# Kernel optimization log

Measured on AMD Instinct MI355X. Metric: run time of the kernel, lower is better.

## Reference

```python
import jax, jax.numpy as jnp
import numpy as np

# dims
B, T, C, D, H, NH, HD, INTER, L = 4, 1024, 256, 256, 512, 8, 64, 2048, 4
CF, CB, BASE = 0, 128, 10000.0  # context_forward, context_backward, rope theta


def _rope_tables():
    inv = 1.0 / (BASE ** (jnp.arange(0, HD, 2, dtype=jnp.float32) / HD))
    t = jnp.arange(T, dtype=jnp.float32)
    f = jnp.einsum('i,j->ij', t, inv)          # [T, HD/2]
    emb = jnp.concatenate([f, f], axis=-1)      # [T, HD]
    return jnp.cos(emb), jnp.sin(emb)


def _rotate_half(x):
    x1, x2 = jnp.split(x, 2, axis=-1)
    return jnp.concatenate([-x2, x1], axis=-1)


def _ln(x, g, b):
    m = x.mean(-1, keepdims=True)
    v = ((x - m) ** 2).mean(-1, keepdims=True)
    return (x - m) / jnp.sqrt(v + 1e-5) * g + b


def _band_mask():
    # create_context_mask(CF, CB, T): allow j in [i-CB, i+CF]
    i = jnp.arange(T)[:, None]
    j = jnp.arange(T)[None, :]
    return (j <= i + CF) & (j >= i - CB)  # [T, T] bool


def setup_inputs() -> dict:
    key = jax.random.key(0)
    ks = jax.random.split(key, 16)
    w = lambda k, shp: (0.02 * jax.random.normal(k, shp)).astype(jnp.float32)
    return {
        'spikes': jax.random.normal(ks[0], (B, T, C), dtype=jnp.float32),
        'spikes_mask': jnp.ones((B, T), dtype=jnp.int32),
        'spikes_timestamp': jnp.tile(jnp.arange(T, dtype=jnp.int32), (B, 1)),
        'embed_w': w(ks[1], (C, D)), 'embed_b': jnp.zeros((D,), jnp.float32),
        'proj_w': w(ks[2], (D, H)), 'proj_b': jnp.zeros((H,), jnp.float32),
        'ln1_g': jnp.ones((L, H), jnp.float32), 'ln1_b': jnp.zeros((L, H), jnp.float32),
        'Wq': w(ks[3], (L, H, H)), 'bq': jnp.zeros((L, H), jnp.float32),
        'Wk': w(ks[4], (L, H, H)), 'bk': jnp.zeros((L, H), jnp.float32),
        'Wv': w(ks[5], (L, H, H)), 'bv': jnp.zeros((L, H), jnp.float32),
        'Wo': w(ks[6], (L, H, H)), 'bo': jnp.zeros((L, H), jnp.float32),
        'ln2_g': jnp.ones((L, H), jnp.float32), 'ln2_b': jnp.zeros((L, H), jnp.float32),
        'up_w': w(ks[7], (L, H, INTER)), 'up_b': jnp.zeros((L, INTER), jnp.float32),
        'down_w': w(ks[8], (L, INTER, H)), 'down_b': jnp.zeros((L, H), jnp.float32),
    }


def reference(spikes, spikes_mask, spikes_timestamp, embed_w, embed_b, proj_w, proj_b,
              ln1_g, ln1_b, Wq, bq, Wk, bk, Wv, bv, Wo, bo, ln2_g, ln2_b,
              up_w, up_b, down_w, down_b):
    cos, sin = _rope_tables()
    mask = _band_mask()[None, None] & (spikes_mask[:, None, None, :] > 0)  # [B,1,T,T]
    cs = cos[spikes_timestamp][:, None]  # [B,1,T,HD]
    sn = sin[spikes_timestamp][:, None]
    neg = jnp.finfo(jnp.float32).min

    # NeuralEmbeddingLayer (no stack/pos/tokens): Linear -> gelu -> Linear
    x = jax.nn.gelu(spikes @ embed_w + embed_b, approximate=False) @ proj_w + proj_b

    for l in range(L):
        h = _ln(x, ln1_g[l], ln1_b[l])
        q = (h @ Wq[l] + bq[l]).reshape(B, T, NH, HD).transpose(0, 2, 1, 3)
        k = (h @ Wk[l] + bk[l]).reshape(B, T, NH, HD).transpose(0, 2, 1, 3)
        v = (h @ Wv[l] + bv[l]).reshape(B, T, NH, HD).transpose(0, 2, 1, 3)
        q = q * cs + _rotate_half(q) * sn
        k = k * cs + _rotate_half(k) * sn
        s = jnp.einsum('bhqd,bhkd->bhqk', q, k) / np.float32(np.sqrt(HD))
        s = jnp.where(mask, s, neg)
        p = jax.nn.softmax(s, axis=-1)
        o = jnp.einsum('bhqk,bhkd->bhqd', p, v).transpose(0, 2, 1, 3).reshape(B, T, H)
        x = x + o @ Wo[l] + bo[l]
        h = _ln(x, ln2_g[l], ln2_b[l])
        x = x + jax.nn.gelu(h @ up_w[l] + up_b[l], approximate=False) @ down_w[l] + down_b[l]
    return x
```

## Files before the change

kernel.cpp:

```cpp
#include <hip/hip_runtime.h>
#include <math.h>

#define B_ 4
#define T_ 1024
#define C_ 256
#define D_ 256
#define H_ 512
#define NH_ 8
#define HD_ 64
#define INTER_ 2048
#define L_ 4
#define CB_ 128

typedef short bf16x8 __attribute__((ext_vector_type(8)));
typedef unsigned short ush8 __attribute__((ext_vector_type(8)));
typedef float f32x4 __attribute__((ext_vector_type(4)));

__device__ __forceinline__ float gelu_exact(float x) {
    return 0.5f * x * (1.0f + erff(x * 0.70710678118654752f));
}

__device__ __forceinline__ unsigned short f2bf(float f) {
    unsigned u = __float_as_uint(f);
    u += 0x7fffu + ((u >> 16) & 1u);
    return (unsigned short)(u >> 16);
}
__device__ __forceinline__ float bf2f(unsigned short h) {
    return __uint_as_float((unsigned)h << 16);
}

__device__ __forceinline__ void xcd_swz(int& bx, int& by) {
    const int gx  = gridDim.x;
    const int nwg = gx * gridDim.y;
    int bid = blockIdx.y * gx + blockIdx.x;
    bid = (bid & 7) * (nwg >> 3) + (bid >> 3);
    bx = bid % gx;
    by = bid / gx;
}

template<int ACT, int RES, int OBF, int SPLIT>
__global__ __launch_bounds__(256) void mm64_k(
    const unsigned short* __restrict__ A, const unsigned short* __restrict__ BT,
    const float* __restrict__ b0, const float* __restrict__ b1,
    const float* __restrict__ b2,
    const float* res,
    void* o0, void* o1, void* o2,
    const int M, const int N, const int K)
{
    __shared__ unsigned short As[64 * 256];
    __shared__ unsigned short Bs[64 * 256];

    int bx, by; xcd_swz(bx, by);

    const int tid  = threadIdx.x;
    const int lane = tid & 63;
    const int w    = tid >> 6;
    const int m0   = by * 64;
    const int n0   = bx * 64;
    const int wm   = (w >> 1) * 32;
    const int wn   = (w & 1) * 32;
    const int l16  = lane & 15;
    const int g16  = lane >> 4;

    f32x4 acc[2][2] = {};

    const unsigned short* Abase = A  + (size_t)m0 * K;
    const unsigned short* Bbase = BT + (size_t)n0 * K;

    for (int k0 = 0; k0 < K; k0 += 256) {
        __syncthreads();
#pragma unroll
        for (int it = 0; it < 8; ++it) {
            const int c  = it * 256 + tid;
            const int rc = c >> 5;
            const int gk = (c & 31) ^ (rc & 7);
            __builtin_amdgcn_global_load_lds(
                (const __attribute__((address_space(1))) unsigned*)(Abase + (size_t)rc * K + k0 + gk * 8),
                (__attribute__((address_space(3))) unsigned*)(As + (size_t)(it * 256 + (w << 6)) * 8), 16, 0, 0);
        }
#pragma unroll
        for (int it = 0; it < 8; ++it) {
            const int c  = it * 256 + tid;
            const int rc = c >> 5;
            const int gk = (c & 31) ^ (rc & 7);
            __builtin_amdgcn_global_load_lds(
                (const __attribute__((address_space(1))) unsigned*)(Bbase + (size_t)rc * K + k0 + gk * 8),
                (__attribute__((address_space(3))) unsigned*)(Bs + (size_t)(it * 256 + (w << 6)) * 8), 16, 0, 0);
        }
        __syncthreads();

#pragma unroll
        for (int kk = 0; kk < 8; ++kk) {
            const int kf = kk * 4 + g16;
            const int sw = (kf ^ (l16 & 7)) * 8;
            bf16x8 a[2], b[2];
#pragma unroll
            for (int t = 0; t < 2; ++t)
                a[t] = *(const bf16x8*)&As[(wm + t * 16 + l16) * 256 + sw];
#pragma unroll
            for (int t = 0; t < 2; ++t)
                b[t] = *(const bf16x8*)&Bs[(wn + t * 16 + l16) * 256 + sw];
#pragma unroll
            for (int i = 0; i < 2; ++i)
#pragma unroll
                for (int j = 0; j < 2; ++j)
                    acc[i][j] = __builtin_amdgcn_mfma_f32_16x16x32_bf16(a[i], b[j], acc[i][j], 0, 0, 0);
        }
    }

    if (OBF || SPLIT) {
        __syncthreads();
        unsigned short* Eb = ((w < 2) ? As : Bs) + (w & 1) * 1024;
        const int row16 = lane >> 2;
        const int cg    = lane & 3;

        const int gnb   = n0 + wn;
        const int which = SPLIT ? (gnb >> 9) : 0;
        const int lnb   = SPLIT ? (gnb & 511) : gnb;
        const int ldo   = SPLIT ? 512 : N;
        unsigned short* oo = SPLIT
            ? ((which == 0) ? (unsigned short*)o0 : (which == 1) ? (unsigned short*)o1 : (unsigned short*)o2)
            : (unsigned short*)o0;
        const float* bb = SPLIT ? ((which == 0) ? b0 : (which == 1) ? b1 : b2) : b0;
        const float scale = (SPLIT && which == 0) ? 0.125f : 1.0f;

#pragma unroll
        for (int i = 0; i < 2; ++i) {
#pragma unroll
            for (int j = 0; j < 2; ++j) {
                const float bv = bb[lnb + j * 16 + l16];
#pragma unroll
                for (int r = 0; r < 4; ++r) {
                    float cv = acc[i][j][r] + bv;
                    if (ACT) cv = gelu_exact(cv);
                    if (SPLIT) cv *= scale;
                    Eb[(g16 * 4 + r) * 40 + j * 16 + l16] = f2bf(cv);
                }
            }
            const int grow0 = m0 + wm + i * 16 + row16;
#pragma unroll
            for (int s = 0; s < 2; ++s) {
                ushort4 t4 = *(const ushort4*)&Eb[row16 * 40 + s * 16 + cg * 4];
                *(ushort4*)&oo[(size_t)grow0 * ldo + lnb + s * 16 + cg * 4] = t4;
            }
        }
        return;
    }

#pragma unroll
    for (int i = 0; i < 2; ++i) {
        const int gmb = m0 + wm + i * 16 + g16 * 4;
#pragma unroll
        for (int j = 0; j < 2; ++j) {
            const int gn = n0 + wn + j * 16 + l16;
            const float bv = b0[gn];
#pragma unroll
            for (int r = 0; r < 4; ++r) {
                float cv = acc[i][j][r] + bv;
                if (ACT) cv = gelu_exact(cv);
                if (RES) cv += res[(size_t)(gmb + r) * 512 + gn];
                ((float*)o0)[(size_t)(gmb + r) * N + gn] = cv;
            }
        }
    }
}

template<int ACT, int RES, int OBF, int SPLIT, int BN>
__global__ __launch_bounds__(256) void mm128_k(
    const unsigned short* __restrict__ A, const unsigned short* __restrict__ BT,
    const float* __restrict__ b0, const float* __restrict__ b1,
    const float* __restrict__ b2,
    const float* res,
    void* o0, void* o1, void* o2,
    const int M, const int N, const int K)
{
    constexpr int NJ = BN / 32;

    __shared__ unsigned short As[128 * 128];
    __shared__ unsigned short Bs[BN * 128];

    int bx, by; xcd_swz(bx, by);

    const int tid  = threadIdx.x;
    const int lane = tid & 63;
    const int w    = tid >> 6;
    const int m0   = by * 128;
    const int n0   = bx * BN;
    const int wm   = (w >> 1) * 64;
    const int wn   = (w & 1) * (BN / 2);
    const int l16  = lane & 15;
    const int g16  = lane >> 4;

    f32x4 acc[4][NJ] = {};

    const unsigned short* Abase = A  + (size_t)m0 * K;
    const unsigned short* Bbase = BT + (size_t)n0 * K;

    for (int k0 = 0; k0 < K; k0 += 128) {
        __syncthreads();
#pragma unroll
        for (int it = 0; it < 8; ++it) {
            const int c  = it * 256 + tid;
            const int rc = c >> 4;
            const int gk = (c & 15) ^ (rc & 7);
            __builtin_amdgcn_global_load_lds(
                (const __attribute__((address_space(1))) unsigned*)(Abase + (size_t)rc * K + k0 + gk * 8),
                (__attribute__((address_space(3))) unsigned*)(As + (size_t)(it * 256 + (w << 6)) * 8), 16, 0, 0);
        }
#pragma unroll
        for (int it = 0; it < NJ * 2; ++it) {
            const int c  = it * 256 + tid;
            const int rc = c >> 4;
            const int gk = (c & 15) ^ (rc & 7);
            __builtin_amdgcn_global_load_lds(
                (const __attribute__((address_space(1))) unsigned*)(Bbase + (size_t)rc * K + k0 + gk * 8),
                (__attribute__((address_space(3))) unsigned*)(Bs + (size_t)(it * 256 + (w << 6)) * 8), 16, 0, 0);
        }
        __syncthreads();

#pragma unroll
        for (int kk = 0; kk < 4; ++kk) {
            const int kf = kk * 4 + g16;
            const int sw = (kf ^ (l16 & 7)) * 8;
            bf16x8 a[4], b[NJ];
#pragma unroll
            for (int t = 0; t < 4; ++t)
                a[t] = *(const bf16x8*)&As[(wm + t * 16 + l16) * 128 + sw];
#pragma unroll
            for (int t = 0; t < NJ; ++t)
                b[t] = *(const bf16x8*)&Bs[(wn + t * 16 + l16) * 128 + sw];
#pragma unroll
            for (int i = 0; i < 4; ++i)
#pragma unroll
                for (int j = 0; j < NJ; ++j)
                    acc[i][j] = __builtin_amdgcn_mfma_f32_16x16x32_bf16(a[i], b[j], acc[i][j], 0, 0, 0);
        }
    }

    if (OBF || SPLIT) {
        __syncthreads();
        constexpr int WC  = NJ * 16;
        constexpr int EST = WC + 8;
        constexpr int LPR = WC / 4;
        constexpr int RPI = 64 / LPR;
        unsigned short* Eb = As + w * (16 * EST);
        const int erow = lane / LPR;
        const int ecol = (lane % LPR) * 4;

        const int gnb   = n0 + wn;
        const int which = SPLIT ? (gnb >> 9) : 0;
        const int lnb   = SPLIT ? (gnb & 511) : gnb;
        const int ldo   = SPLIT ? 512 : N;
        unsigned short* oo = SPLIT
            ? ((which == 0) ? (unsigned short*)o0 : (which == 1) ? (unsigned short*)o1 : (unsigned short*)o2)
            : (unsigned short*)o0;
        const float* bb = SPLIT ? ((which == 0) ? b0 : (which == 1) ? b1 : b2) : b0;
        const float scale = (SPLIT && which == 0) ? 0.125f : 1.0f;

#pragma unroll
        for (int i = 0; i < 4; ++i) {
#pragma unroll
            for (int j = 0; j < NJ; ++j) {
                const float bv = bb[lnb + j * 16 + l16];
#pragma unroll
                for (int r = 0; r < 4; ++r) {
                    float cv = acc[i][j][r] + bv;
                    if (ACT) cv = gelu_exact(cv);
                    if (SPLIT) cv *= scale;
                    Eb[(g16 * 4 + r) * EST + j * 16 + l16] = f2bf(cv);
                }
            }
            const int grow0 = m0 + wm + i * 16;
#pragma unroll
            for (int s = 0; s < NJ; ++s) {
                ushort4 t4 = *(const ushort4*)&Eb[(s * RPI + erow) * EST + ecol];
                *(ushort4*)&oo[(size_t)(grow0 + s * RPI + erow) * ldo + lnb + ecol] = t4;
            }
        }
        return;
    }

#pragma unroll
    for (int i = 0; i < 4; ++i) {
        const int gmb = m0 + wm + i * 16 + g16 * 4;
#pragma unroll
        for (int j = 0; j < NJ; ++j) {
            const int gn = n0 + wn + j * 16 + l16;
            const float bv = b0[gn];
#pragma unroll
            for (int r = 0; r < 4; ++r) {
                float cv = acc[i][j][r] + bv;
                if (ACT) cv = gelu_exact(cv);
                if (RES) cv += res[(size_t)(gmb + r) * 512 + gn];
                ((float*)o0)[(size_t)(gmb + r) * N + gn] = cv;
            }
        }
    }
}

__global__ __launch_bounds__(256) void prep_k(
    const float* __restrict__ spikes,
    const float* __restrict__ embed_w, const float* __restrict__ proj_w,
    const float* __restrict__ Wq, const float* __restrict__ Wk,
    const float* __restrict__ Wv, const float* __restrict__ Wo,
    const float* __restrict__ up_w, const float* __restrict__ down_w,
    const int* __restrict__ ts,
    unsigned short* __restrict__ spbf,
    unsigned short* __restrict__ embT, unsigned short* __restrict__ projT,
    unsigned short* __restrict__ qkvT, unsigned short* __restrict__ woT,
    unsigned short* __restrict__ upT, unsigned short* __restrict__ downT,
    float2* __restrict__ rope_tab)
{
    const int idx = blockIdx.x;
    const int tid = threadIdx.x;

    if (idx >= 3376) {
        const int e0 = (idx - 3376) * 4096 + tid * 16;
#pragma unroll
        for (int i = 0; i < 16; ++i) {
            const int e = e0 + i;
            const int row = e >> 5, d = e & 31;
            const float tstamp = (float)ts[row];
            const float freq = __expf(-0.2878231366242558f * (float)d);
            const float ang = tstamp * freq;
            rope_tab[e] = make_float2(__cosf(ang), __sinf(ang));
        }
        return;
    }

    if (idx >= 3120) {
        const int base = (idx - 3120) * 4096 + tid * 16;
#pragma unroll
        for (int s = 0; s < 4; ++s) {
            float4 v = *(const float4*)&spikes[base + s * 4];
            ushort4 o = {f2bf(v.x), f2bf(v.y), f2bf(v.z), f2bf(v.w)};
            *(ushort4*)&spbf[base + s * 4] = o;
        }
        return;
    }

    const float* src; unsigned short* dst; int R, Cc, t;
    if (idx < 16)      { src = embed_w; dst = embT;  R = C_; Cc = D_; t = idx; }
    else if (idx < 48) { src = proj_w;  dst = projT; R = D_; Cc = H_; t = idx - 16; }
    else if (idx < 816) {
        const int j = idx - 48;
        const int wsel = j >> 8;
        const int l = (j & 255) >> 6;
        t = j & 63;
        src = ((wsel == 0) ? Wq : (wsel == 1) ? Wk : Wv) + (size_t)l * H_ * H_;
        dst = qkvT + (size_t)l * 3 * H_ * H_ + (size_t)wsel * H_ * H_;
        R = H_; Cc = H_;
    } else if (idx < 1072) {
        const int j = idx - 816; const int l = j >> 6; t = j & 63;
        src = Wo + (size_t)l * H_ * H_; dst = woT + (size_t)l * H_ * H_;
        R = H_; Cc = H_;
    } else if (idx < 2096) {
        const int j = idx - 1072; const int l = j >> 8; t = j & 255;
        src = up_w + (size_t)l * H_ * INTER_; dst = upT + (size_t)l * INTER_ * H_;
        R = H_; Cc = INTER_;
    } else {
        const int j = idx - 2096; const int l = j >> 8; t = j & 255;
        src = down_w + (size_t)l * INTER_ * H_; dst = downT + (size_t)l * H_ * INTER_;
        R = INTER_; Cc = H_;
    }
    const int ntx = Cc >> 6;
    const int c0 = (t % ntx) * 64, r0 = (t / ntx) * 64;

    __shared__ float tile[64][65];
    const int tr = tid >> 4, tc = (tid & 15) * 4;
#pragma unroll
    for (int i = 0; i < 4; ++i) {
        float4 v = *(const float4*)&src[(size_t)(r0 + tr + i * 16) * Cc + c0 + tc];
        tile[tr + i * 16][tc + 0] = v.x;
        tile[tr + i * 16][tc + 1] = v.y;
        tile[tr + i * 16][tc + 2] = v.z;
        tile[tr + i * 16][tc + 3] = v.w;
    }
    __syncthreads();
#pragma unroll
    for (int i = 0; i < 4; ++i) {
        const int n = tr + i * 16;
        ushort4 o;
        o.x = f2bf(tile[tc + 0][n]);
        o.y = f2bf(tile[tc + 1][n]);
        o.z = f2bf(tile[tc + 2][n]);
        o.w = f2bf(tile[tc + 3][n]);
        *(ushort4*)&dst[(size_t)(c0 + n) * R + r0 + tc] = o;
    }
}

__global__ __launch_bounds__(256) void ln_k(
    const float* __restrict__ x, const float* __restrict__ g,
    const float* __restrict__ b, unsigned short* __restrict__ out)
{
    const int wave = threadIdx.x >> 6;
    const int lane = threadIdx.x & 63;
    const int row  = blockIdx.x * 4 + wave;
    const float* xr = x + (size_t)row * H_;
    const int c0 = lane * 8;

    float4 a0 = *(const float4*)&xr[c0];
    float4 a1 = *(const float4*)&xr[c0 + 4];

    float s = a0.x + a0.y + a0.z + a0.w + a1.x + a1.y + a1.z + a1.w;
#pragma unroll
    for (int off = 32; off; off >>= 1) s += __shfl_xor(s, off);
    const float mean = s * (1.0f / (float)H_);

    float d[8];
    d[0] = a0.x - mean; d[1] = a0.y - mean; d[2] = a0.z - mean; d[3] = a0.w - mean;
    d[4] = a1.x - mean; d[5] = a1.y - mean; d[6] = a1.z - mean; d[7] = a1.w - mean;
    float q = 0.0f;
#pragma unroll
    for (int j = 0; j < 8; ++j) q += d[j] * d[j];
#pragma unroll
    for (int off = 32; off; off >>= 1) q += __shfl_xor(q, off);
    const float rstd = rsqrtf(q * (1.0f / (float)H_) + 1e-5f);

    float4 g0 = *(const float4*)&g[c0];
    float4 g1 = *(const float4*)&g[c0 + 4];
    float4 b0 = *(const float4*)&b[c0];
    float4 b1 = *(const float4*)&b[c0 + 4];

    ushort4 o0, o1;
    o0.x = f2bf(d[0] * rstd * g0.x + b0.x);
    o0.y = f2bf(d[1] * rstd * g0.y + b0.y);
    o0.z = f2bf(d[2] * rstd * g0.z + b0.z);
    o0.w = f2bf(d[3] * rstd * g0.w + b0.w);
    o1.x = f2bf(d[4] * rstd * g1.x + b1.x);
    o1.y = f2bf(d[5] * rstd * g1.y + b1.y);
    o1.z = f2bf(d[6] * rstd * g1.z + b1.z);
    o1.w = f2bf(d[7] * rstd * g1.w + b1.w);
    *(ushort4*)&out[(size_t)row * H_ + c0]     = o0;
    *(ushort4*)&out[(size_t)row * H_ + c0 + 4] = o1;
}

#define AWIN 192
#define AKS 72
#define AVS 200

__global__ __launch_bounds__(256) void attn_k(
    const unsigned short* __restrict__ q, const unsigned short* __restrict__ k,
    const unsigned short* __restrict__ v, const int* __restrict__ smask,
    const float2* __restrict__ rope_tab, unsigned short* __restrict__ o)
{
    __shared__ unsigned short Ks[AWIN * AKS];
    __shared__ unsigned short Vt[64 * AVS];
    unsigned short* const Pb = Ks;

    const int blk = blockIdx.x;
    const int qt = blk & 15;
    const int h  = (blk >> 4) & 7;
    const int b  = blk >> 7;
    const int tid  = threadIdx.x;
    const int lane = tid & 63;
    const int w    = tid >> 6;
    const int l16  = lane & 15;
    const int g16  = lane >> 4;

    const int qlo = qt * 64;
    const int klo = (qlo >= CB_) ? (qlo - CB_) : 0;
    const int tb  = b * 1024;

    bf16x8 qa0, qa1;
    {
        const int qrow = w * 16 + l16;
        const unsigned short* gq = q + ((size_t)(tb + qlo + qrow)) * 512 + h * 64;
        ush8 lo = *(const ush8*)&gq[g16 * 8];
        ush8 hi = *(const ush8*)&gq[g16 * 8 + 32];
        const float2* tr = rope_tab + (size_t)(tb + qlo + qrow) * 32 + g16 * 8;
#pragma unroll
        for (int j = 0; j < 8; ++j) {
            const float2 cs = tr[j];
            const float v1 = bf2f(lo[j]);
            const float v2 = bf2f(hi[j]);
            ((unsigned short*)&qa0)[j] = f2bf(v1 * cs.x - v2 * cs.y);
            ((unsigned short*)&qa1)[j] = f2bf(v2 * cs.x + v1 * cs.y);
        }
    }

    {
        const unsigned short* gk = k + ((size_t)(tb + klo)) * 512 + h * 64;
        for (int c = tid; c < AWIN * 8; c += 256) {
            const int row = c >> 3, c4 = (c & 7) * 4;
            ushort4 lo = *(const ushort4*)&gk[(size_t)row * 512 + c4];
            ushort4 hi = *(const ushort4*)&gk[(size_t)row * 512 + c4 + 32];
            const float2* tr = rope_tab + (size_t)(tb + klo + row) * 32 + c4;
            ushort4 olo, ohi;
#pragma unroll
            for (int j2 = 0; j2 < 4; ++j2) {
                const float2 cs = tr[j2];
                const float v1 = bf2f(((const unsigned short*)&lo)[j2]);
                const float v2 = bf2f(((const unsigned short*)&hi)[j2]);
                ((unsigned short*)&olo)[j2] = f2bf(v1 * cs.x - v2 * cs.y);
                ((unsigned short*)&ohi)[j2] = f2bf(v2 * cs.x + v1 * cs.y);
            }
            *(ushort4*)&Ks[row * AKS + c4]      = olo;
            *(ushort4*)&Ks[row * AKS + c4 + 32] = ohi;
        }
    }
    {
        const unsigned short* gv = v + ((size_t)(tb + klo)) * 512 + h * 64;
        for (int c = tid; c < AWIN * 16; c += 256) {
            const int row = c >> 4, c4 = (c & 15) * 4;
            ushort4 vv = *(const ushort4*)&gv[(size_t)row * 512 + c4];
            Vt[(c4 + 0) * AVS + row] = vv.x;
            Vt[(c4 + 1) * AVS + row] = vv.y;
            Vt[(c4 + 2) * AVS + row] = vv.z;
            Vt[(c4 + 3) * AVS + row] = vv.w;
        }
    }
    __syncthreads();

    f32x4 accs[12];
#pragma unroll
    for (int t = 0; t < 12; ++t) {
        const bf16x8 b0 = *(const bf16x8*)&Ks[(t * 16 + l16) * AKS + g16 * 8];
        const bf16x8 b1 = *(const bf16x8*)&Ks[(t * 16 + l16) * AKS + 32 + g16 * 8];
        f32x4 c = {};
        c = __builtin_amdgcn_mfma_f32_16x16x32_bf16(qa0, b0, c, 0, 0, 0);
        c = __builtin_amdgcn_mfma_f32_16x16x32_bf16(qa1, b1, c, 0, 0, 0);
        accs[t] = c;
    }

    bool mk[12];
    int  jj[12];
#pragma unroll
    for (int t = 0; t < 12; ++t) {
        jj[t] = klo + t * 16 + l16;
        mk[t] = smask[tb + jj[t]] > 0;
    }

    float rs[4];
#pragma unroll
    for (int r = 0; r < 4; ++r) {
        const int i = qlo + 16 * w + g16 * 4 + r;
        float mx = -1e30f;
#pragma unroll
        for (int t = 0; t < 12; ++t) {
            const bool val = mk[t] && (jj[t] >= i - CB_) && (jj[t] <= i);
            mx = fmaxf(mx, val ? accs[t][r] : -1e30f);
        }
        mx = fmaxf(mx, __shfl_xor(mx, 1));
        mx = fmaxf(mx, __shfl_xor(mx, 2));
        mx = fmaxf(mx, __shfl_xor(mx, 4));
        mx = fmaxf(mx, __shfl_xor(mx, 8));
        float sum = 0.0f;
#pragma unroll
        for (int t = 0; t < 12; ++t) {
            const bool val = mk[t] && (jj[t] >= i - CB_) && (jj[t] <= i);
            const float p = val ? __expf(accs[t][r] - mx) : 0.0f;
            accs[t][r] = p;
            sum += p;
        }
        sum += __shfl_xor(sum, 1);
        sum += __shfl_xor(sum, 2);
        sum += __shfl_xor(sum, 4);
        sum += __shfl_xor(sum, 8);
        rs[r] = 1.0f / sum;
    }

    __syncthreads();

#pragma unroll
    for (int t = 0; t < 12; ++t)
#pragma unroll
        for (int r = 0; r < 4; ++r)
            Pb[(16 * w + g16 * 4 + r) * AVS + t * 16 + l16] = f2bf(accs[t][r]);

    f32x4 acco[4];
#pragma unroll
    for (int nt = 0; nt < 4; ++nt) {
        f32x4 c = {};
#pragma unroll
        for (int ks = 0; ks < 6; ++ks) {
            const bf16x8 a = *(const bf16x8*)&Pb[(16 * w + l16) * AVS + ks * 32 + g16 * 8];
            const bf16x8 bb = *(const bf16x8*)&Vt[(nt * 16 + l16) * AVS + ks * 32 + g16 * 8];
            c = __builtin_amdgcn_mfma_f32_16x16x32_bf16(a, bb, c, 0, 0, 0);
        }
        acco[nt] = c;
    }

    __syncthreads();
#pragma unroll
    for (int nt = 0; nt < 4; ++nt)
#pragma unroll
        for (int r = 0; r < 4; ++r)
            Pb[(16 * w + g16 * 4 + r) * AVS + nt * 16 + l16] = f2bf(acco[nt][r] * rs[r]);

    const int row16 = lane >> 2, cg = lane & 3;
    const int grow = tb + qlo + 16 * w + row16;
#pragma unroll
    for (int s = 0; s < 4; ++s) {
        ushort4 t4 = *(const ushort4*)&Pb[(16 * w + row16) * AVS + s * 16 + cg * 4];
        *(ushort4*)&o[(size_t)grow * 512 + h * 64 + s * 16 + cg * 4] = t4;
    }
}

extern "C" void kernel_launch(void* const* d_in, const int* in_sizes, int n_in,
                              void* d_out, int out_size, void* d_ws, size_t ws_size,
                              hipStream_t stream)
{
    const float* spikes  = (const float*)d_in[0];
    const int*   smask   = (const int*)d_in[1];
    const int*   ts      = (const int*)d_in[2];
    const float* embed_w = (const float*)d_in[3];
    const float* embed_b = (const float*)d_in[4];
    const float* proj_w  = (const float*)d_in[5];
    const float* proj_b  = (const float*)d_in[6];
    const float* ln1_g   = (const float*)d_in[7];
    const float* ln1_b   = (const float*)d_in[8];
    const float* Wq      = (const float*)d_in[9];
    const float* bq      = (const float*)d_in[10];
    const float* Wk      = (const float*)d_in[11];
    const float* bk      = (const float*)d_in[12];
    const float* Wv      = (const float*)d_in[13];
    const float* bv      = (const float*)d_in[14];
    const float* Wo      = (const float*)d_in[15];
    const float* bo      = (const float*)d_in[16];
    const float* ln2_g   = (const float*)d_in[17];
    const float* ln2_b   = (const float*)d_in[18];
    const float* up_w    = (const float*)d_in[19];
    const float* up_b    = (const float*)d_in[20];
    const float* down_w  = (const float*)d_in[21];
    const float* down_b  = (const float*)d_in[22];

    const int M = B_ * T_;

    char* p = (char*)d_ws;
    float* x = (float*)p;                       p += (size_t)M * H_ * 4;
    unsigned short* qb  = (unsigned short*)p;   p += (size_t)M * H_ * 2;
    unsigned short* kb  = (unsigned short*)p;   p += (size_t)M * H_ * 2;
    unsigned short* vb  = (unsigned short*)p;   p += (size_t)M * H_ * 2;
    unsigned short* hbf = (unsigned short*)p;   p += (size_t)M * H_ * 2;
    unsigned short* obf = (unsigned short*)p;   p += (size_t)M * H_ * 2;
    unsigned short* ibf = (unsigned short*)p;   p += (size_t)M * INTER_ * 2;
    unsigned short* tbf = (unsigned short*)p;   p += (size_t)M * D_ * 2;
    unsigned short* spbf  = (unsigned short*)p; p += (size_t)M * C_ * 2;
    unsigned short* embT  = (unsigned short*)p; p += (size_t)D_ * C_ * 2;
    unsigned short* projT = (unsigned short*)p; p += (size_t)H_ * D_ * 2;
    unsigned short* qkvT  = (unsigned short*)p; p += (size_t)L_ * 3 * H_ * H_ * 2;
    unsigned short* woT   = (unsigned short*)p; p += (size_t)L_ * H_ * H_ * 2;
    unsigned short* upT   = (unsigned short*)p; p += (size_t)L_ * INTER_ * H_ * 2;
    unsigned short* downT = (unsigned short*)p; p += (size_t)L_ * H_ * INTER_ * 2;
    float2* rope_tab = (float2*)p;              p += (size_t)M * 32 * sizeof(float2);

    prep_k<<<3408, 256, 0, stream>>>(
        spikes, embed_w, proj_w, Wq, Wk, Wv, Wo, up_w, down_w, ts,
        spbf, embT, projT, qkvT, woT, upT, downT, rope_tab);

    mm64_k<1, 0, 1, 0><<<dim3(D_ / 64, M / 64), 256, 0, stream>>>(
        spbf, embT, embed_b, nullptr, nullptr, nullptr,
        tbf, nullptr, nullptr, M, D_, C_);
    mm64_k<0, 0, 0, 0><<<dim3(H_ / 64, M / 64), 256, 0, stream>>>(
        tbf, projT, proj_b, nullptr, nullptr, nullptr,
        x, nullptr, nullptr, M, H_, D_);

    for (int l = 0; l < L_; ++l) {
        const unsigned short* qkvT_l = qkvT + (size_t)l * 3 * H_ * H_;
        const unsigned short* woT_l  = woT  + (size_t)l * H_ * H_;
        const unsigned short* upT_l  = upT  + (size_t)l * INTER_ * H_;
        const unsigned short* dnT_l  = downT + (size_t)l * H_ * INTER_;

        ln_k<<<M / 4, 256, 0, stream>>>(x, ln1_g + l * H_, ln1_b + l * H_, hbf);

        mm128_k<0, 0, 1, 1, 64><<<dim3((3 * H_) / 64, M / 128), 256, 0, stream>>>(
            hbf, qkvT_l, bq + l * H_, bk + l * H_, bv + l * H_, nullptr,
            qb, kb, vb, M, 3 * H_, H_);

        attn_k<<<B_ * NH_ * (T_ / 64), 256, 0, stream>>>(qb, kb, vb, smask,
                                                         rope_tab, obf);

        mm64_k<0, 1, 0, 0><<<dim3(H_ / 64, M / 64), 256, 0, stream>>>(
            obf, woT_l, bo + l * H_, nullptr, nullptr, x,
            x, nullptr, nullptr, M, H_, H_);

        ln_k<<<M / 4, 256, 0, stream>>>(x, ln2_g + l * H_, ln2_b + l * H_, hbf);

        mm128_k<1, 0, 1, 0, 128><<<dim3(INTER_ / 128, M / 128), 256, 0, stream>>>(
            hbf, upT_l, up_b + l * INTER_, nullptr, nullptr, nullptr,
            ibf, nullptr, nullptr, M, INTER_, H_);

        float* dst = (l == L_ - 1) ? (float*)d_out : x;
        mm64_k<0, 1, 0, 0><<<dim3(H_ / 64, M / 64), 256, 0, stream>>>(
            ibf, dnT_l, down_b + l * H_, nullptr, nullptr, x,
            dst, nullptr, nullptr, M, H_, INTER_);
    }
}
```

Measured before the change: 483.5 us.

## Fuse RoPE into QKV GEMM epilogue and drop it from attention

RoPE is now applied in the QKV projection epilogue. Each warp is remapped to own 32 rows by all 64 columns of a head, so the rotate-half partner columns sit in the same thread's accumulators. The attention kernel then loads already-rotated Q and K straight from global memory, skipping the per-block rotation and the rope table reads. This removes RoPE work that was repeated across overlapping attention windows, at the cost of a different warp tiling and more epilogue work in the QKV GEMM.

```diff
diff --git a/kernel.cpp b/kernel.cpp
--- a/kernel.cpp
+++ b/kernel.cpp
@@ -38,13 +38,12 @@
     by = bid / gx;
 }
 
-template<int ACT, int RES, int OBF, int SPLIT>
+template<int ACT, int RES, int OBF>
 __global__ __launch_bounds__(256) void mm64_k(
     const unsigned short* __restrict__ A, const unsigned short* __restrict__ BT,
-    const float* __restrict__ b0, const float* __restrict__ b1,
-    const float* __restrict__ b2,
+    const float* __restrict__ b0,
     const float* res,
-    void* o0, void* o1, void* o2,
+    void* o0,
     const int M, const int N, const int K)
 {
     __shared__ unsigned short As[64 * 256];
@@ -108,32 +107,21 @@
         }
     }
 
-    if (OBF || SPLIT) {
+    if (OBF) {
         __syncthreads();
         unsigned short* Eb = ((w < 2) ? As : Bs) + (w & 1) * 1024;
         const int row16 = lane >> 2;
         const int cg    = lane & 3;
 
-        const int gnb   = n0 + wn;
-        const int which = SPLIT ? (gnb >> 9) : 0;
-        const int lnb   = SPLIT ? (gnb & 511) : gnb;
-        const int ldo   = SPLIT ? 512 : N;
-        unsigned short* oo = SPLIT
-            ? ((which == 0) ? (unsigned short*)o0 : (which == 1) ? (unsigned short*)o1 : (unsigned short*)o2)
-            : (unsigned short*)o0;
-        const float* bb = SPLIT ? ((which == 0) ? b0 : (which == 1) ? b1 : b2) : b0;
-        const float scale = (SPLIT && which == 0) ? 0.125f : 1.0f;
-
 #pragma unroll
         for (int i = 0; i < 2; ++i) {
 #pragma unroll
             for (int j = 0; j < 2; ++j) {
-                const float bv = bb[lnb + j * 16 + l16];
+                const float bv = b0[n0 + wn + j * 16 + l16];
 #pragma unroll
                 for (int r = 0; r < 4; ++r) {
                     float cv = acc[i][j][r] + bv;
                     if (ACT) cv = gelu_exact(cv);
-                    if (SPLIT) cv *= scale;
                     Eb[(g16 * 4 + r) * 40 + j * 16 + l16] = f2bf(cv);
                 }
             }
@@ -141,7 +129,7 @@
 #pragma unroll
             for (int s = 0; s < 2; ++s) {
                 ushort4 t4 = *(const ushort4*)&Eb[row16 * 40 + s * 16 + cg * 4];
-                *(ushort4*)&oo[(size_t)grow0 * ldo + lnb + s * 16 + cg * 4] = t4;
+                *(ushort4*)&((unsigned short*)o0)[(size_t)grow0 * N + n0 + wn + s * 16 + cg * 4] = t4;
             }
         }
         return;
@@ -165,16 +153,17 @@
     }
 }
 
-template<int ACT, int RES, int OBF, int SPLIT, int BN>
+template<int ACT, int OBF, int SPLIT, int BN>
 __global__ __launch_bounds__(256) void mm128_k(
     const unsigned short* __restrict__ A, const unsigned short* __restrict__ BT,
     const float* __restrict__ b0, const float* __restrict__ b1,
     const float* __restrict__ b2,
-    const float* res,
+    const float2* __restrict__ rope_tab,
     void* o0, void* o1, void* o2,
     const int M, const int N, const int K)
 {
-    constexpr int NJ = BN / 32;
+    constexpr int NI = SPLIT ? 2 : 4;
+    constexpr int NJ = SPLIT ? 4 : (BN / 32);
 
     __shared__ unsigned short As[128 * 128];
     __shared__ unsigned short Bs[BN * 128];
@@ -186,12 +175,12 @@
     const int w    = tid >> 6;
     const int m0   = by * 128;
     const int n0   = bx * BN;
-    const int wm   = (w >> 1) * 64;
-    const int wn   = (w & 1) * (BN / 2);
+    const int wm   = SPLIT ? (w * 32) : ((w >> 1) * 64);
+    const int wn   = SPLIT ? 0 : ((w & 1) * (BN / 2));
     const int l16  = lane & 15;
     const int g16  = lane >> 4;
 
-    f32x4 acc[4][NJ] = {};
+    f32x4 acc[NI][NJ] = {};
 
     const unsigned short* Abase = A  + (size_t)m0 * K;
     const unsigned short* Bbase = BT + (size_t)n0 * K;
@@ -208,7 +197,7 @@
                 (__attribute__((address_space(3))) unsigned*)(As + (size_t)(it * 256 + (w << 6)) * 8), 16, 0, 0);
         }
 #pragma unroll
-        for (int it = 0; it < NJ * 2; ++it) {
+        for (int it = 0; it < (BN / 128) * 8 + (BN == 64 ? 4 : 0); ++it) {
             const int c  = it * 256 + tid;
             const int rc = c >> 4;
             const int gk = (c & 15) ^ (rc & 7);
@@ -222,22 +211,69 @@
         for (int kk = 0; kk < 4; ++kk) {
             const int kf = kk * 4 + g16;
             const int sw = (kf ^ (l16 & 7)) * 8;
-            bf16x8 a[4], b[NJ];
-#pragma unroll
-            for (int t = 0; t < 4; ++t)
+            bf16x8 a[NI], b[NJ];
+#pragma unroll
+            for (int t = 0; t < NI; ++t)
                 a[t] = *(const bf16x8*)&As[(wm + t * 16 + l16) * 128 + sw];
 #pragma unroll
             for (int t = 0; t < NJ; ++t)
                 b[t] = *(const bf16x8*)&Bs[(wn + t * 16 + l16) * 128 + sw];
 #pragma unroll
-            for (int i = 0; i < 4; ++i)
+            for (int i = 0; i < NI; ++i)
 #pragma unroll
                 for (int j = 0; j < NJ; ++j)
                     acc[i][j] = __builtin_amdgcn_mfma_f32_16x16x32_bf16(a[i], b[j], acc[i][j], 0, 0, 0);
         }
     }
 
-    if (OBF || SPLIT) {
+    if (SPLIT) {
+        __syncthreads();
+        constexpr int EST = 72;
+        unsigned short* Eb = As + w * (16 * EST);
+        const int erow = lane >> 4;
+        const int ecol = (lane & 15) * 4;
+
+        const int which = n0 >> 9;
+        const int lnb   = n0 & 511;
+        unsigned short* oo = (which == 0) ? (unsigned short*)o0
+                           : (which == 1) ? (unsigned short*)o1 : (unsigned short*)o2;
+        const float* bb = (which == 0) ? b0 : (which == 1) ? b1 : b2;
+        const float scale = (which == 0) ? 0.125f : 1.0f;
+        const bool doRope = (which <= 1);
+
+#pragma unroll
+        for (int i = 0; i < 2; ++i) {
+            const int r0g = m0 + w * 32 + i * 16;
+#pragma unroll
+            for (int j = 0; j < 2; ++j) {
+                const int d = j * 16 + l16;
+                const float bv1 = bb[lnb + d];
+                const float bv2 = bb[lnb + d + 32];
+#pragma unroll
+                for (int r = 0; r < 4; ++r) {
+                    float v1 = acc[i][j][r]     + bv1;
+                    float v2 = acc[i][j + 2][r] + bv2;
+                    float u1 = v1, u2 = v2;
+                    if (doRope) {
+                        const int row = r0g + g16 * 4 + r;
+                        const float2 cs = rope_tab[(size_t)row * 32 + d];
+                        u1 = v1 * cs.x - v2 * cs.y;
+                        u2 = v2 * cs.x + v1 * cs.y;
+                    }
+                    Eb[(g16 * 4 + r) * EST + d]      = f2bf(u1 * scale);
+                    Eb[(g16 * 4 + r) * EST + d + 32] = f2bf(u2 * scale);
+                }
+            }
+#pragma unroll
+            for (int s = 0; s < 4; ++s) {
+                ushort4 t4 = *(const ushort4*)&Eb[(s * 4 + erow) * EST + ecol];
+                *(ushort4*)&oo[(size_t)(r0g + s * 4 + erow) * 512 + lnb + ecol] = t4;
+            }
+        }
+        return;
+    }
+
+    if (OBF) {
         __syncthreads();
         constexpr int WC  = NJ * 16;
         constexpr int EST = WC + 8;
@@ -247,26 +283,15 @@
         const int erow = lane / LPR;
         const int ecol = (lane % LPR) * 4;
 
-        const int gnb   = n0 + wn;
-        const int which = SPLIT ? (gnb >> 9) : 0;
-        const int lnb   = SPLIT ? (gnb & 511) : gnb;
-        const int ldo   = SPLIT ? 512 : N;
-        unsigned short* oo = SPLIT
-            ? ((which == 0) ? (unsigned short*)o0 : (which == 1) ? (unsigned short*)o1 : (unsigned short*)o2)
-            : (unsigned short*)o0;
-        const float* bb = SPLIT ? ((which == 0) ? b0 : (which == 1) ? b1 : b2) : b0;
-        const float scale = (SPLIT && which == 0) ? 0.125f : 1.0f;
-
-#pragma unroll
-        for (int i = 0; i < 4; ++i) {
+#pragma unroll
+        for (int i = 0; i < NI; ++i) {
 #pragma unroll
             for (int j = 0; j < NJ; ++j) {
-                const float bv = bb[lnb + j * 16 + l16];
+                const float bv = b0[n0 + wn + j * 16 + l16];
 #pragma unroll
                 for (int r = 0; r < 4; ++r) {
                     float cv = acc[i][j][r] + bv;
                     if (ACT) cv = gelu_exact(cv);
-                    if (SPLIT) cv *= scale;
                     Eb[(g16 * 4 + r) * EST + j * 16 + l16] = f2bf(cv);
                 }
             }
@@ -274,14 +299,14 @@
 #pragma unroll
             for (int s = 0; s < NJ; ++s) {
                 ushort4 t4 = *(const ushort4*)&Eb[(s * RPI + erow) * EST + ecol];
-                *(ushort4*)&oo[(size_t)(grow0 + s * RPI + erow) * ldo + lnb + ecol] = t4;
+                *(ushort4*)&((unsigned short*)o0)[(size_t)(grow0 + s * RPI + erow) * N + n0 + wn + ecol] = t4;
             }
         }
         return;
     }
 
 #pragma unroll
-    for (int i = 0; i < 4; ++i) {
+    for (int i = 0; i < NI; ++i) {
         const int gmb = m0 + wm + i * 16 + g16 * 4;
 #pragma unroll
         for (int j = 0; j < NJ; ++j) {
@@ -291,7 +316,6 @@
             for (int r = 0; r < 4; ++r) {
                 float cv = acc[i][j][r] + bv;
                 if (ACT) cv = gelu_exact(cv);
-                if (RES) cv += res[(size_t)(gmb + r) * 512 + gn];
                 ((float*)o0)[(size_t)(gmb + r) * N + gn] = cv;
             }
         }
@@ -442,7 +466,7 @@
 __global__ __launch_bounds__(256) void attn_k(
     const unsigned short* __restrict__ q, const unsigned short* __restrict__ k,
     const unsigned short* __restrict__ v, const int* __restrict__ smask,
-    const float2* __restrict__ rope_tab, unsigned short* __restrict__ o)
+    unsigned short* __restrict__ o)
 {
     __shared__ unsigned short Ks[AWIN * AKS];
     __shared__ unsigned short Vt[64 * AVS];
@@ -466,37 +490,16 @@
     {
         const int qrow = w * 16 + l16;
         const unsigned short* gq = q + ((size_t)(tb + qlo + qrow)) * 512 + h * 64;
-        ush8 lo = *(const ush8*)&gq[g16 * 8];
-        ush8 hi = *(const ush8*)&gq[g16 * 8 + 32];
-        const float2* tr = rope_tab + (size_t)(tb + qlo + qrow) * 32 + g16 * 8;
-#pragma unroll
-        for (int j = 0; j < 8; ++j) {
-            const float2 cs = tr[j];
-            const float v1 = bf2f(lo[j]);
-            const float v2 = bf2f(hi[j]);
-            ((unsigned short*)&qa0)[j] = f2bf(v1 * cs.x - v2 * cs.y);
-            ((unsigned short*)&qa1)[j] = f2bf(v2 * cs.x + v1 * cs.y);
-        }
+        qa0 = *(const bf16x8*)&gq[g16 * 8];
+        qa1 = *(const bf16x8*)&gq[g16 * 8 + 32];
     }
 
     {
         const unsigned short* gk = k + ((size_t)(tb + klo)) * 512 + h * 64;
         for (int c = tid; c < AWIN * 8; c += 256) {
-            const int row = c >> 3, c4 = (c & 7) * 4;
-            ushort4 lo = *(const ushort4*)&gk[(size_t)row * 512 + c4];
-            ushort4 hi = *(const ushort4*)&gk[(size_t)row * 512 + c4 + 32];
-            const float2* tr = rope_tab + (size_t)(tb + klo + row) * 32 + c4;
-            ushort4 olo, ohi;
-#pragma unroll
-            for (int j2 = 0; j2 < 4; ++j2) {
-                const float2 cs = tr[j2];
-                const float v1 = bf2f(((const unsigned short*)&lo)[j2]);
-                const float v2 = bf2f(((const unsigned short*)&hi)[j2]);
-                ((unsigned short*)&olo)[j2] = f2bf(v1 * cs.x - v2 * cs.y);
-                ((unsigned short*)&ohi)[j2] = f2bf(v2 * cs.x + v1 * cs.y);
-            }
-            *(ushort4*)&Ks[row * AKS + c4]      = olo;
-            *(ushort4*)&Ks[row * AKS + c4 + 32] = ohi;
+            const int row = c >> 3, ch = (c & 7) * 8;
+            ush8 v8 = *(const ush8*)&gk[(size_t)row * 512 + ch];
+            *(ush8*)&Ks[row * AKS + ch] = v8;
         }
     }
     {
@@ -649,12 +652,10 @@
         spikes, embed_w, proj_w, Wq, Wk, Wv, Wo, up_w, down_w, ts,
         spbf, embT, projT, qkvT, woT, upT, downT, rope_tab);
 
-    mm64_k<1, 0, 1, 0><<<dim3(D_ / 64, M / 64), 256, 0, stream>>>(
-        spbf, embT, embed_b, nullptr, nullptr, nullptr,
-        tbf, nullptr, nullptr, M, D_, C_);
-    mm64_k<0, 0, 0, 0><<<dim3(H_ / 64, M / 64), 256, 0, stream>>>(
-        tbf, projT, proj_b, nullptr, nullptr, nullptr,
-        x, nullptr, nullptr, M, H_, D_);
+    mm64_k<1, 0, 1><<<dim3(D_ / 64, M / 64), 256, 0, stream>>>(
+        spbf, embT, embed_b, nullptr, tbf, M, D_, C_);
+    mm64_k<0, 0, 0><<<dim3(H_ / 64, M / 64), 256, 0, stream>>>(
+        tbf, projT, proj_b, nullptr, x, M, H_, D_);
 
     for (int l = 0; l < L_; ++l) {
         const unsigned short* qkvT_l = qkvT + (size_t)l * 3 * H_ * H_;
@@ -664,26 +665,23 @@
 
         ln_k<<<M / 4, 256, 0, stream>>>(x, ln1_g + l * H_, ln1_b + l * H_, hbf);
 
-        mm128_k<0, 0, 1, 1, 64><<<dim3((3 * H_) / 64, M / 128), 256, 0, stream>>>(
-            hbf, qkvT_l, bq + l * H_, bk + l * H_, bv + l * H_, nullptr,
+        mm128_k<0, 0, 1, 64><<<dim3((3 * H_) / 64, M / 128), 256, 0, stream>>>(
+            hbf, qkvT_l, bq + l * H_, bk + l * H_, bv + l * H_, rope_tab,
             qb, kb, vb, M, 3 * H_, H_);
 
-        attn_k<<<B_ * NH_ * (T_ / 64), 256, 0, stream>>>(qb, kb, vb, smask,
-                                                         rope_tab, obf);
-
-        mm64_k<0, 1, 0, 0><<<dim3(H_ / 64, M / 64), 256, 0, stream>>>(
-            obf, woT_l, bo + l * H_, nullptr, nullptr, x,
-            x, nullptr, nullptr, M, H_, H_);
+        attn_k<<<B_ * NH_ * (T_ / 64), 256, 0, stream>>>(qb, kb, vb, smask, obf);
+
+        mm64_k<0, 1, 0><<<dim3(H_ / 64, M / 64), 256, 0, stream>>>(
+            obf, woT_l, bo + l * H_, x, x, M, H_, H_);
 
         ln_k<<<M / 4, 256, 0, stream>>>(x, ln2_g + l * H_, ln2_b + l * H_, hbf);
 
-        mm128_k<1, 0, 1, 0, 128><<<dim3(INTER_ / 128, M / 128), 256, 0, stream>>>(
+        mm128_k<1, 1, 0, 128><<<dim3(INTER_ / 128, M / 128), 256, 0, stream>>>(
             hbf, upT_l, up_b + l * INTER_, nullptr, nullptr, nullptr,
             ibf, nullptr, nullptr, M, INTER_, H_);
 
         float* dst = (l == L_ - 1) ? (float*)d_out : x;
-        mm64_k<0, 1, 0, 0><<<dim3(H_ / 64, M / 64), 256, 0, stream>>>(
-            ibf, dnT_l, down_b + l * H_, nullptr, nullptr, x,
-            dst, nullptr, nullptr, M, H_, INTER_);
-    }
-}
+        mm64_k<0, 1, 0><<<dim3(H_ / 64, M / 64), 256, 0, stream>>>(
+            ibf, dnT_l, down_b + l * H_, x, dst, M, H_, INTER_);
+    }
+}
```

After: 491.4 us. About the same (+1.6%).
